# Optimization experiments

Hardware: AMD Instinct MI355X
Metric: run time of the kernel (lower is better)

Reference implementation:

```python
import jax, jax.numpy as jnp
import numpy as np

B, N, D, H, F = 2, 2048, 512, 8, 8
HD = D // H

def setup_inputs() -> dict:
    key = jax.random.key(0)
    ks = jax.random.split(key, 11)
    s = 1.0 / np.sqrt(D)
    return {
        "x": jax.random.normal(ks[0], (B, N, D), dtype=jnp.float32),
        "phase_coords": jax.random.uniform(ks[1], (B, N, F), dtype=jnp.float32) * 6.28,
        "Wq": jax.random.normal(ks[2], (D, D), dtype=jnp.float32) * s,
        "bq": jax.random.normal(ks[3], (D,), dtype=jnp.float32) * 0.01,
        "Wk": jax.random.normal(ks[4], (D, D), dtype=jnp.float32) * s,
        "bk": jax.random.normal(ks[5], (D,), dtype=jnp.float32) * 0.01,
        "Wv": jax.random.normal(ks[6], (D, D), dtype=jnp.float32) * s,
        "bv": jax.random.normal(ks[7], (D,), dtype=jnp.float32) * 0.01,
        "Wo": jax.random.normal(ks[8], (D, D), dtype=jnp.float32) * s,
        "bo": jax.random.normal(ks[9], (D,), dtype=jnp.float32) * 0.01,
        "phase_bias": jax.random.normal(ks[10], (H, F), dtype=jnp.float32) * 0.1,
    }

def reference(x, phase_coords, Wq, bq, Wk, bk, Wv, bv, Wo, bo, phase_bias):
    b, n, _ = x.shape
    def proj(W, bias):
        # [B,N,D] -> [B,H,N,HD]
        return (x @ W.T + bias).reshape(b, n, H, HD).transpose(0, 2, 1, 3)
    Q, K, V = proj(Wq, bq), proj(Wk, bk), proj(Wv, bv)
    scores = jnp.einsum("bhqd,bhkd->bhqk", Q, K) / np.sqrt(HD)
    # phase coherence bias: cos of pairwise phase diffs, weighted per head
    phase_diff = phase_coords[:, :, None, :] - phase_coords[:, None, :, :]  # [B,N,N,F]
    coherence = jnp.cos(phase_diff)
    bias = jnp.einsum("bqkf,hf->bhqk", coherence, phase_bias)
    scores = scores + bias
    attn = jax.nn.softmax(scores, axis=-1)
    attended = jnp.einsum("bhqk,bhkd->bhqd", attn, V)
    attended = attended.transpose(0, 2, 1, 3).reshape(b, n, D)
    return attended @ Wo.T + bo
```

## Files before the change

### kernel.cpp

```cpp
#include <hip/hip_runtime.h>
#include <stdint.h>

typedef unsigned short u16;
typedef unsigned int   u32;
typedef __bf16 bf16x8 __attribute__((ext_vector_type(8)));
typedef float  f32x4  __attribute__((ext_vector_type(4)));
typedef u16    u16x8  __attribute__((ext_vector_type(8)));
typedef u16    u16x4  __attribute__((ext_vector_type(4)));

#define B_  2
#define N_  2048
#define D_  512
#define H_  8
#define HD_ 64
#define QKD 96
#define LOG2E 1.4426950408889634f

__device__ __forceinline__ u16 f2bf(float f) {
  union { float f; u32 u; } v; v.f = f;
  u32 r = v.u + 0x7FFFu + ((v.u >> 16) & 1u);
  return (u16)(r >> 16);
}
__device__ __forceinline__ u16 f2bf_trunc(float f) {
  union { float f; u32 u; } v; v.f = f;
  return (u16)(v.u >> 16);
}
__device__ __forceinline__ void gload_lds16(const void* g, void* l) {
  __builtin_amdgcn_global_load_lds(
      (const __attribute__((address_space(1))) void*)g,
      (__attribute__((address_space(3))) void*)l, 16, 0, 0);
}

__global__ __launch_bounds__(256) void k_prep(
    const float* __restrict__ x, const float* __restrict__ pc,
    const float* __restrict__ Wq, const float* __restrict__ bq,
    const float* __restrict__ Wk, const float* __restrict__ bk,
    const float* __restrict__ Wv, const float* __restrict__ bv,
    const float* __restrict__ Wo, const float* __restrict__ pb,
    u16* __restrict__ xb, u16* __restrict__ wqkvb, float* __restrict__ bqkv,
    u16* __restrict__ wob, u16* __restrict__ Qe, u16* __restrict__ Ke)
{
  int gid = blockIdx.x * blockDim.x + threadIdx.x;
  int stride = gridDim.x * blockDim.x;
  const float qs = 0.125f * LOG2E;
  for (int i = gid; i < B_ * N_ * D_; i += stride) xb[i] = f2bf(x[i]);
  for (int i = gid; i < 3 * D_ * D_; i += stride) {
    int r = i >> 9;
    float v;
    if (r < 512)       v = Wq[i] * qs;
    else if (r < 1024) v = Wk[i - 512 * 512];
    else               v = Wv[i - 1024 * 512];
    wqkvb[i] = f2bf(v);
  }
  for (int i = gid; i < 3 * D_; i += stride) {
    float v;
    if (i < 512)       v = bq[i] * qs;
    else if (i < 1024) v = bk[i - 512];
    else               v = bv[i - 1024];
    bqkv[i] = v;
  }
  for (int i = gid; i < D_ * D_; i += stride) wob[i] = f2bf(Wo[i]);

  for (int i = gid; i < 16 * N_ * 4; i += stride) {
    int idx = i >> 2, part = i & 3;
    int bh = idx >> 11, n = idx & 2047;
    int b = bh >> 3, h = bh & 7;
    size_t base = ((size_t)bh * N_ + n) * QKD + 64 + part * 8;
    u16x8 qv, kv;
    if (part < 2) {
#pragma unroll
      for (int f = 0; f < 8; f++) {
        float a = pc[((size_t)b * N_ + n) * 8 + f];
        float t = (part == 0) ? __cosf(a) : __sinf(a);
        kv[f] = f2bf(t);
        qv[f] = f2bf(pb[h * 8 + f] * LOG2E * t);
      }
    } else {
#pragma unroll
      for (int f = 0; f < 8; f++) { qv[f] = 0; kv[f] = 0; }
    }
    *(u16x8*)&Qe[base] = qv;
    *(u16x8*)&Ke[base] = kv;
  }
}

template <int MODE, int BN>
__global__ __launch_bounds__(256) void k_gemm(
    const u16* __restrict__ A, const u16* __restrict__ Bm,
    const float* __restrict__ bias,
    u16* __restrict__ Qe, u16* __restrict__ Ke, u16* __restrict__ Vt,
    float* __restrict__ Of)
{
  constexpr int JT  = BN / 32;
  constexpr int BNC = BN / 32;
  __shared__ u16 As[3][64 * 64];
  __shared__ u16 Bs[3][BN * 64];
  const int tid = threadIdx.x;
  const int wave = tid >> 6, lane = tid & 63;
  const int fr = lane & 15, kg = lane >> 4;
  const int m0 = blockIdx.x * 64, n0 = blockIdx.y * BN;
  const int wr = (wave >> 1) * 32, wc = (wave & 1) * (BN / 2);

  f32x4 acc[2][JT];
#pragma unroll
  for (int i = 0; i < 2; i++)
#pragma unroll
    for (int j = 0; j < JT; j++)
#pragma unroll
      for (int r = 0; r < 4; r++) acc[i][j][r] = 0.f;

  auto stage = [&](int buf, int k0) {
#pragma unroll
    for (int u = 0; u < 2; u++) {
      int chunk = (wave * 2 + u) * 64 + lane;
      int row = chunk >> 3, cl = chunk & 7;
      gload_lds16(A + (size_t)(m0 + row) * 512 + k0 + ((cl ^ (row & 7)) << 3),
                  &As[buf][(wave * 2 + u) * 512]);
    }
#pragma unroll
    for (int u = 0; u < BNC; u++) {
      int chunk = (wave * BNC + u) * 64 + lane;
      int row = chunk >> 3, cl = chunk & 7;
      gload_lds16(Bm + (size_t)(n0 + row) * 512 + k0 + ((cl ^ (row & 7)) << 3),
                  &Bs[buf][(wave * BNC + u) * 512]);
    }
  };

  stage(0, 0);
  stage(1, 64);

#pragma unroll
  for (int s = 0; s < 8; s++) {
    if (s < 7) {
      if constexpr (BN == 128) asm volatile("s_waitcnt vmcnt(6)" ::: "memory");
      else                     asm volatile("s_waitcnt vmcnt(4)" ::: "memory");
    } else {
      asm volatile("s_waitcnt vmcnt(0)" ::: "memory");
    }
    asm volatile("s_waitcnt lgkmcnt(0)" ::: "memory");
    __builtin_amdgcn_sched_barrier(0);
    __builtin_amdgcn_s_barrier();
    __builtin_amdgcn_sched_barrier(0);
    if (s < 6) stage((s + 2) % 3, (s + 2) * 64);
    const int cb = s % 3;
#pragma unroll
    for (int ksub = 0; ksub < 2; ksub++) {
      bf16x8 af[2], bf[JT];
#pragma unroll
      for (int i = 0; i < 2; i++)
        af[i] = *(const bf16x8*)&As[cb][(wr + i * 16 + fr) * 64 + (((ksub * 4 + kg) ^ (fr & 7)) << 3)];
#pragma unroll
      for (int j = 0; j < JT; j++)
        bf[j] = *(const bf16x8*)&Bs[cb][(wc + j * 16 + fr) * 64 + (((ksub * 4 + kg) ^ (fr & 7)) << 3)];
#pragma unroll
      for (int i = 0; i < 2; i++)
#pragma unroll
        for (int j = 0; j < JT; j++)
          acc[i][j] = __builtin_amdgcn_mfma_f32_16x16x32_bf16(af[i], bf[j], acc[i][j], 0, 0, 0);
    }
  }

  if (MODE == 1) {
#pragma unroll
    for (int j = 0; j < JT; j++) {
      int col = n0 + wc + j * 16 + fr;
      float bc = bias[col];
#pragma unroll
      for (int i = 0; i < 2; i++)
#pragma unroll
        for (int r = 0; r < 4; r++)
          Of[(size_t)(m0 + wr + i * 16 + kg * 4 + r) * 512 + col] = acc[i][j][r] + bc;
  } } else {
    const int seg = n0 >> 9;
    const int nb = n0 & 511;
    if (seg < 2) {
      u16* dst = seg ? Ke : Qe;
#pragma unroll
      for (int j = 0; j < JT; j++) {
        int col = nb + wc + j * 16 + fr;
        float bc = bias[n0 + wc + j * 16 + fr];
        int h = col >> 6, d = col & 63;
#pragma unroll
        for (int i = 0; i < 2; i++) {
#pragma unroll
          for (int r = 0; r < 4; r++) {
            int row = m0 + wr + i * 16 + kg * 4 + r;
            int b = row >> 11, nn = row & 2047;
            dst[((size_t)(b * 8 + h) * N_ + nn) * QKD + d] = f2bf(acc[i][j][r] + bc);
          }
        }
      }
    } else {
#pragma unroll
      for (int j = 0; j < JT; j++) {
        int cc = nb + wc + j * 16 + fr;
        float bc = bias[n0 + wc + j * 16 + fr];
        int h = cc >> 6, d = cc & 63;
#pragma unroll
        for (int i = 0; i < 2; i++) {
          int row = m0 + wr + i * 16 + kg * 4;
          int b = row >> 11, n = row & 2047;
          u16x4 o;
#pragma unroll
          for (int r = 0; r < 4; r++) o[r] = f2bf(acc[i][j][r] + bc);
          *(u16x4*)&Vt[((size_t)(b * 8 + h) * 64 + d) * N_ + n] = o;
        }
      }
    }
  }
}

__global__ __launch_bounds__(256, 3) void k_attn(
    const u16* __restrict__ Qe, const u16* __restrict__ Ke,
    const u16* __restrict__ Vt, u16* __restrict__ attb)
{
  const int bh = blockIdx.x, b = bh >> 3, h = bh & 7;
  const int q0 = blockIdx.y * 128;
  const int tid = threadIdx.x, wave = tid >> 6, lane = tid & 63;
  const int fr = lane & 15, kg = lane >> 4;

  __shared__ u16 Klds[2][64 * 96];
  __shared__ u16 Vlds[2][64 * 64];
  __shared__ u16 Plds[4][32 * 64];

  auto stageK = [&](int buf, int kv) {
#pragma unroll
    for (int p = 0; p < 3; p++) {
      u32 c = p * 256 + tid;
      u32 r = c / 12u, s = c - r * 12u;
      u32 g = (s < 8) ? (s ^ (r & 7)) : (8 + ((s & 3) ^ (r & 3)));
      gload_lds16(Ke + ((size_t)bh * N_ + kv + r) * QKD + g * 8,
                  &Klds[buf][(p * 256 + wave * 64) * 8]);
    }
  };
  auto stageV = [&](int buf, int kv) {
#pragma unroll
    for (int p = 0; p < 2; p++) {
      int c = p * 256 + tid;
      int row = c >> 3, c8 = c & 7;
      gload_lds16(Vt + ((size_t)bh * 64 + row) * N_ + kv + ((c8 ^ (row & 7)) << 3),
                  &Vlds[buf][(p * 256 + wave * 64) * 8]);
    }
  };

  bf16x8 qa[2][3];
#pragma unroll
  for (int i = 0; i < 2; i++) {
    size_t gq = (size_t)bh * N_ + q0 + wave * 32 + i * 16 + fr;
#pragma unroll
    for (int ks = 0; ks < 3; ks++)
      qa[i][ks] = *(const bf16x8*)&Qe[gq * QKD + ks * 32 + kg * 8];
  }

  f32x4 accO[2][4];
#pragma unroll
  for (int i = 0; i < 2; i++)
#pragma unroll
    for (int d = 0; d < 4; d++)
#pragma unroll
      for (int r = 0; r < 4; r++) accO[i][d][r] = 0.f;
  float Lacc[2][4];
#pragma unroll
  for (int i = 0; i < 2; i++)
#pragma unroll
    for (int r = 0; r < 4; r++) Lacc[i][r] = 0.f;

  stageK(0, 0);
  stageV(0, 0);
  stageK(1, 64);
  stageV(1, 64);

  for (int t = 0; t < 32; t++) {
    const int cb = t & 1;
    if (t < 31) asm volatile("s_waitcnt vmcnt(5)" ::: "memory");
    else        asm volatile("s_waitcnt vmcnt(0)" ::: "memory");
    __builtin_amdgcn_sched_barrier(0);
    __builtin_amdgcn_s_barrier();
    __builtin_amdgcn_sched_barrier(0);

    f32x4 accS[2][4];
#pragma unroll
    for (int i = 0; i < 2; i++)
#pragma unroll
      for (int j = 0; j < 4; j++)
#pragma unroll
        for (int r = 0; r < 4; r++) accS[i][j][r] = 0.f;

    __builtin_amdgcn_s_setprio(1);
#pragma unroll
    for (int ks = 0; ks < 3; ks++) {
#pragma unroll
      for (int j = 0; j < 4; j++) {
        int slot = (ks < 2) ? ((ks * 4 + kg) ^ (fr & 7)) : (8 + (kg ^ (fr & 3)));
        bf16x8 kb = *(const bf16x8*)&Klds[cb][(j * 16 + fr) * 96 + slot * 8];
#pragma unroll
        for (int i = 0; i < 2; i++)
          accS[i][j] = __builtin_amdgcn_mfma_f32_16x16x32_bf16(qa[i][ks], kb, accS[i][j], 0, 0, 0);
      }
    }
    __builtin_amdgcn_s_setprio(0);

#pragma unroll
    for (int i = 0; i < 2; i++) {
#pragma unroll
      for (int j = 0; j < 4; j++) {
#pragma unroll
        for (int r = 0; r < 4; r++) {
          float p = __builtin_amdgcn_exp2f(accS[i][j][r] - 11.5415603f);
          Lacc[i][r] += p;
          int rw = i * 16 + kg * 4 + r;
          Plds[wave][rw * 64 + ((j * 16 + fr) ^ ((rw & 7) << 3))] = f2bf_trunc(p);
        }
      }
    }
    asm volatile("s_waitcnt lgkmcnt(0)" ::: "memory");
    __builtin_amdgcn_sched_barrier(0);

    __builtin_amdgcn_s_setprio(1);
#pragma unroll
    for (int ks = 0; ks < 2; ks++) {
      bf16x8 pa[2];
#pragma unroll
      for (int i = 0; i < 2; i++)
        pa[i] = *(const bf16x8*)&Plds[wave][(i * 16 + fr) * 64 + ((ks * 32 + kg * 8) ^ ((fr & 7) << 3))];
#pragma unroll
      for (int d = 0; d < 4; d++) {
        bf16x8 vb = *(const bf16x8*)&Vlds[cb][(d * 16 + fr) * 64 + (((ks * 4 + kg) ^ (fr & 7)) << 3)];
#pragma unroll
        for (int i = 0; i < 2; i++)
          accO[i][d] = __builtin_amdgcn_mfma_f32_16x16x32_bf16(pa[i], vb, accO[i][d], 0, 0, 0);
      }
    }
    __builtin_amdgcn_s_setprio(0);

    __builtin_amdgcn_sched_barrier(0);
    __builtin_amdgcn_s_barrier();
    __builtin_amdgcn_sched_barrier(0);
    if (t + 2 < 32) {
      stageV(cb, (t + 2) * 64);
      stageK(cb, (t + 2) * 64);
    }
  }

#pragma unroll
  for (int i = 0; i < 2; i++) {
#pragma unroll
    for (int r = 0; r < 4; r++) {
      float l = Lacc[i][r];
      l += __shfl_xor(l, 1); l += __shfl_xor(l, 2);
      l += __shfl_xor(l, 4); l += __shfl_xor(l, 8);
      float inv = 1.0f / l;
      int qg = q0 + wave * 32 + i * 16 + kg * 4 + r;
#pragma unroll
      for (int d = 0; d < 4; d++)
        attb[(size_t)(b * N_ + qg) * 512 + h * 64 + d * 16 + fr] = f2bf(accO[i][d][r] * inv);
    }
  }
}

extern "C" void kernel_launch(void* const* d_in, const int* in_sizes, int n_in,
                              void* d_out, int out_size, void* d_ws, size_t ws_size,
                              hipStream_t stream)
{
  (void)in_sizes; (void)n_in; (void)out_size; (void)ws_size;
  const float* x  = (const float*)d_in[0];
  const float* pc = (const float*)d_in[1];
  const float* Wq = (const float*)d_in[2];
  const float* bq = (const float*)d_in[3];
  const float* Wk = (const float*)d_in[4];
  const float* bk = (const float*)d_in[5];
  const float* Wv = (const float*)d_in[6];
  const float* bv = (const float*)d_in[7];
  const float* Wo = (const float*)d_in[8];
  const float* bo = (const float*)d_in[9];
  const float* pb = (const float*)d_in[10];

  u16* ws = (u16*)d_ws;
  const size_t TOK = (size_t)B_ * N_;
  u16* xb    = ws;
  u16* Qe    = xb    + TOK * D_;
  u16* Ke    = Qe    + (size_t)16 * N_ * QKD;
  u16* Vt    = Ke    + (size_t)16 * N_ * QKD;
  u16* attb  = Vt    + TOK * D_;
  u16* wqkvb = attb  + TOK * D_;
  u16* wob   = wqkvb + (size_t)3 * D_ * D_;
  float* bqkv = (float*)(wob + (size_t)D_ * D_);

  k_prep<<<1024, 256, 0, stream>>>(x, pc, Wq, bq, Wk, bk, Wv, bv, Wo, pb,
                                   xb, wqkvb, bqkv, wob, Qe, Ke);
  k_gemm<0, 128><<<dim3(64, 12), 256, 0, stream>>>(xb, wqkvb, bqkv, Qe, Ke, Vt, nullptr);
  k_attn<<<dim3(16, 16), 256, 0, stream>>>(Qe, Ke, Vt, attb);
  k_gemm<1, 64><<<dim3(64, 8), 256, 0, stream>>>(attb, wob, bo, nullptr, nullptr, nullptr, (float*)d_out);
}
```

Baseline: 158.9 us.

## Split attention across 8 waves with 16 query rows each; remap GEMM tiles per XCD

The attention kernel now runs 512 threads per block, with each of the 8 waves owning 16 query rows instead of 4 waves owning 32. K/V staging is redistributed over the larger block, and the vmcnt waits are adjusted per wave to match the new load count. The GEMM kernels switch to a 1D grid with a swizzled tile mapping so that consecutive tiles land on the same XCD (blockIdx mod 8), aiming for better L2 reuse. The attention change halves per-wave register use and adds latency hiding. In exchange, each K/V tile loaded into LDS now feeds fewer MFMAs per wave, and the larger block adds barrier cost.

```diff
diff --git a/kernel.cpp b/kernel.cpp
--- a/kernel.cpp
+++ b/kernel.cpp
@@ -93,12 +93,16 @@
 {
   constexpr int JT  = BN / 32;
   constexpr int BNC = BN / 32;
+  constexpr int NT  = (MODE == 0 ? 1536 : 512) / BN;
+  constexpr int CHUNK = 64 * NT / 8;
   __shared__ u16 As[3][64 * 64];
   __shared__ u16 Bs[3][BN * 64];
   const int tid = threadIdx.x;
   const int wave = tid >> 6, lane = tid & 63;
   const int fr = lane & 15, kg = lane >> 4;
-  const int m0 = blockIdx.x * 64, n0 = blockIdx.y * BN;
+  const int g = blockIdx.x;
+  const int T = (g & 7) * CHUNK + (g >> 3);
+  const int m0 = (T / NT) * 64, n0 = (T % NT) * BN;
   const int wr = (wave >> 1) * 32, wc = (wave & 1) * (BN / 2);
 
   f32x4 acc[2][JT];
@@ -210,7 +214,7 @@
   }
 }
 
-__global__ __launch_bounds__(256, 3) void k_attn(
+__global__ __launch_bounds__(512) void k_attn(
     const u16* __restrict__ Qe, const u16* __restrict__ Ke,
     const u16* __restrict__ Vt, u16* __restrict__ attb)
 {
@@ -221,49 +225,45 @@
 
   __shared__ u16 Klds[2][64 * 96];
   __shared__ u16 Vlds[2][64 * 64];
-  __shared__ u16 Plds[4][32 * 64];
+  __shared__ u16 Plds[8][16 * 64];
 
   auto stageK = [&](int buf, int kv) {
-#pragma unroll
-    for (int p = 0; p < 3; p++) {
-      u32 c = p * 256 + tid;
+    {
+      u32 c = tid;
       u32 r = c / 12u, s = c - r * 12u;
       u32 g = (s < 8) ? (s ^ (r & 7)) : (8 + ((s & 3) ^ (r & 3)));
       gload_lds16(Ke + ((size_t)bh * N_ + kv + r) * QKD + g * 8,
-                  &Klds[buf][(p * 256 + wave * 64) * 8]);
+                  &Klds[buf][(wave * 64) * 8]);
+    }
+    if (tid < 256) {
+      u32 c = 512 + tid;
+      u32 r = c / 12u, s = c - r * 12u;
+      u32 g = (s < 8) ? (s ^ (r & 7)) : (8 + ((s & 3) ^ (r & 3)));
+      gload_lds16(Ke + ((size_t)bh * N_ + kv + r) * QKD + g * 8,
+                  &Klds[buf][(512 + wave * 64) * 8]);
     }
   };
   auto stageV = [&](int buf, int kv) {
-#pragma unroll
-    for (int p = 0; p < 2; p++) {
-      int c = p * 256 + tid;
-      int row = c >> 3, c8 = c & 7;
-      gload_lds16(Vt + ((size_t)bh * 64 + row) * N_ + kv + ((c8 ^ (row & 7)) << 3),
-                  &Vlds[buf][(p * 256 + wave * 64) * 8]);
-    }
+    int c = tid;
+    int row = c >> 3, c8 = c & 7;
+    gload_lds16(Vt + ((size_t)bh * 64 + row) * N_ + kv + ((c8 ^ (row & 7)) << 3),
+                &Vlds[buf][(wave * 64) * 8]);
   };
 
-  bf16x8 qa[2][3];
-#pragma unroll
-  for (int i = 0; i < 2; i++) {
-    size_t gq = (size_t)bh * N_ + q0 + wave * 32 + i * 16 + fr;
+  bf16x8 qa[3];
+  {
+    size_t gq = (size_t)bh * N_ + q0 + wave * 16 + fr;
 #pragma unroll
     for (int ks = 0; ks < 3; ks++)
-      qa[i][ks] = *(const bf16x8*)&Qe[gq * QKD + ks * 32 + kg * 8];
-  }
-
-  f32x4 accO[2][4];
-#pragma unroll
-  for (int i = 0; i < 2; i++)
-#pragma unroll
-    for (int d = 0; d < 4; d++)
-#pragma unroll
-      for (int r = 0; r < 4; r++) accO[i][d][r] = 0.f;
-  float Lacc[2][4];
-#pragma unroll
-  for (int i = 0; i < 2; i++)
-#pragma unroll
-    for (int r = 0; r < 4; r++) Lacc[i][r] = 0.f;
+      qa[ks] = *(const bf16x8*)&Qe[gq * QKD + ks * 32 + kg * 8];
+  }
+
+  f32x4 accO[4];
+#pragma unroll
+  for (int d = 0; d < 4; d++)
+#pragma unroll
+    for (int r = 0; r < 4; r++) accO[d][r] = 0.f;
+  float Lacc[4] = {0.f, 0.f, 0.f, 0.f};
 
   stageK(0, 0);
   stageV(0, 0);
@@ -272,19 +272,21 @@
 
   for (int t = 0; t < 32; t++) {
     const int cb = t & 1;
-    if (t < 31) asm volatile("s_waitcnt vmcnt(5)" ::: "memory");
-    else        asm volatile("s_waitcnt vmcnt(0)" ::: "memory");
+    if (t < 31) {
+      if (wave < 4) asm volatile("s_waitcnt vmcnt(3)" ::: "memory");
+      else          asm volatile("s_waitcnt vmcnt(2)" ::: "memory");
+    } else {
+      asm volatile("s_waitcnt vmcnt(0)" ::: "memory");
+    }
     __builtin_amdgcn_sched_barrier(0);
     __builtin_amdgcn_s_barrier();
     __builtin_amdgcn_sched_barrier(0);
 
-    f32x4 accS[2][4];
-#pragma unroll
-    for (int i = 0; i < 2; i++)
-#pragma unroll
-      for (int j = 0; j < 4; j++)
-#pragma unroll
-        for (int r = 0; r < 4; r++) accS[i][j][r] = 0.f;
+    f32x4 accS[4];
+#pragma unroll
+    for (int j = 0; j < 4; j++)
+#pragma unroll
+      for (int r = 0; r < 4; r++) accS[j][r] = 0.f;
 
     __builtin_amdgcn_s_setprio(1);
 #pragma unroll
@@ -293,24 +295,19 @@
       for (int j = 0; j < 4; j++) {
         int slot = (ks < 2) ? ((ks * 4 + kg) ^ (fr & 7)) : (8 + (kg ^ (fr & 3)));
         bf16x8 kb = *(const bf16x8*)&Klds[cb][(j * 16 + fr) * 96 + slot * 8];
-#pragma unroll
-        for (int i = 0; i < 2; i++)
-          accS[i][j] = __builtin_amdgcn_mfma_f32_16x16x32_bf16(qa[i][ks], kb, accS[i][j], 0, 0, 0);
+        accS[j] = __builtin_amdgcn_mfma_f32_16x16x32_bf16(qa[ks], kb, accS[j], 0, 0, 0);
       }
     }
     __builtin_amdgcn_s_setprio(0);
 
 #pragma unroll
-    for (int i = 0; i < 2; i++) {
-#pragma unroll
-      for (int j = 0; j < 4; j++) {
-#pragma unroll
-        for (int r = 0; r < 4; r++) {
-          float p = __builtin_amdgcn_exp2f(accS[i][j][r] - 11.5415603f);
-          Lacc[i][r] += p;
-          int rw = i * 16 + kg * 4 + r;
-          Plds[wave][rw * 64 + ((j * 16 + fr) ^ ((rw & 7) << 3))] = f2bf_trunc(p);
-        }
+    for (int j = 0; j < 4; j++) {
+#pragma unroll
+      for (int r = 0; r < 4; r++) {
+        float p = __builtin_amdgcn_exp2f(accS[j][r] - 11.5415603f);
+        Lacc[r] += p;
+        int rw = kg * 4 + r;
+        Plds[wave][rw * 64 + ((j * 16 + fr) ^ ((rw & 7) << 3))] = f2bf_trunc(p);
       }
     }
     asm volatile("s_waitcnt lgkmcnt(0)" ::: "memory");
@@ -319,16 +316,11 @@
     __builtin_amdgcn_s_setprio(1);
 #pragma unroll
     for (int ks = 0; ks < 2; ks++) {
-      bf16x8 pa[2];
-#pragma unroll
-      for (int i = 0; i < 2; i++)
-        pa[i] = *(const bf16x8*)&Plds[wave][(i * 16 + fr) * 64 + ((ks * 32 + kg * 8) ^ ((fr & 7) << 3))];
+      bf16x8 pa = *(const bf16x8*)&Plds[wave][fr * 64 + ((ks * 32 + kg * 8) ^ ((fr & 7) << 3))];
 #pragma unroll
       for (int d = 0; d < 4; d++) {
         bf16x8 vb = *(const bf16x8*)&Vlds[cb][(d * 16 + fr) * 64 + (((ks * 4 + kg) ^ (fr & 7)) << 3)];
-#pragma unroll
-        for (int i = 0; i < 2; i++)
-          accO[i][d] = __builtin_amdgcn_mfma_f32_16x16x32_bf16(pa[i], vb, accO[i][d], 0, 0, 0);
+        accO[d] = __builtin_amdgcn_mfma_f32_16x16x32_bf16(pa, vb, accO[d], 0, 0, 0);
       }
     }
     __builtin_amdgcn_s_setprio(0);
@@ -343,18 +335,15 @@
   }
 
 #pragma unroll
-  for (int i = 0; i < 2; i++) {
-#pragma unroll
-    for (int r = 0; r < 4; r++) {
-      float l = Lacc[i][r];
-      l += __shfl_xor(l, 1); l += __shfl_xor(l, 2);
-      l += __shfl_xor(l, 4); l += __shfl_xor(l, 8);
-      float inv = 1.0f / l;
-      int qg = q0 + wave * 32 + i * 16 + kg * 4 + r;
-#pragma unroll
-      for (int d = 0; d < 4; d++)
-        attb[(size_t)(b * N_ + qg) * 512 + h * 64 + d * 16 + fr] = f2bf(accO[i][d][r] * inv);
-    }
+  for (int r = 0; r < 4; r++) {
+    float l = Lacc[r];
+    l += __shfl_xor(l, 1); l += __shfl_xor(l, 2);
+    l += __shfl_xor(l, 4); l += __shfl_xor(l, 8);
+    float inv = 1.0f / l;
+    int qg = q0 + wave * 16 + kg * 4 + r;
+#pragma unroll
+    for (int d = 0; d < 4; d++)
+      attb[(size_t)(b * N_ + qg) * 512 + h * 64 + d * 16 + fr] = f2bf(accO[d][r] * inv);
   }
 }
 
@@ -388,7 +377,7 @@
 
   k_prep<<<1024, 256, 0, stream>>>(x, pc, Wq, bq, Wk, bk, Wv, bv, Wo, pb,
                                    xb, wqkvb, bqkv, wob, Qe, Ke);
-  k_gemm<0, 128><<<dim3(64, 12), 256, 0, stream>>>(xb, wqkvb, bqkv, Qe, Ke, Vt, nullptr);
-  k_attn<<<dim3(16, 16), 256, 0, stream>>>(Qe, Ke, Vt, attb);
-  k_gemm<1, 64><<<dim3(64, 8), 256, 0, stream>>>(attb, wob, bo, nullptr, nullptr, nullptr, (float*)d_out);
-}
+  k_gemm<0, 128><<<768, 256, 0, stream>>>(xb, wqkvb, bqkv, Qe, Ke, Vt, nullptr);
+  k_attn<<<dim3(16, 16), 512, 0, stream>>>(Qe, Ke, Vt, attb);
+  k_gemm<1, 64><<<512, 256, 0, stream>>>(attb, wob, bo, nullptr, nullptr, nullptr, (float*)d_out);
+}
```

Result: faster. 151.9 us (-4.4%).
